# Optimization experiments

Hardware: AMD Instinct MI355X
Metric: run time of the kernel (lower is better)

## Reference

```python
import jax, jax.numpy as jnp
import numpy as np

B, T0, F, H, G = 32, 50, 171, 1024, 300


def _lstm_cell(x, h, c, Wih, Whh, bih, bhh):
    # PyTorch LSTMCell: gates ordered i, f, g, o
    gates = x @ Wih.T + bih + h @ Whh.T + bhh
    i, f, g, o = jnp.split(gates, 4, axis=-1)
    c_new = jax.nn.sigmoid(f) * c + jax.nn.sigmoid(i) * jnp.tanh(g)
    h_new = jax.nn.sigmoid(o) * jnp.tanh(c_new)
    return h_new, c_new


def setup_inputs() -> dict:
    key = jax.random.key(0)
    ks = jax.random.split(key, 16)
    s = 0.03  # small init to avoid gate saturation over 350 steps
    inp = {
        "initial_seq": jax.random.normal(ks[0], (B, T0, F), jnp.float32),
        "generate_frames_number": G,
        "Wih1": jax.random.normal(ks[1], (4 * H, F), jnp.float32) * s,
        "Whh1": jax.random.normal(ks[2], (4 * H, H), jnp.float32) * s,
        "bih1": jax.random.normal(ks[3], (4 * H,), jnp.float32) * s,
        "bhh1": jax.random.normal(ks[4], (4 * H,), jnp.float32) * s,
        "Wih2": jax.random.normal(ks[5], (4 * H, H), jnp.float32) * s,
        "Whh2": jax.random.normal(ks[6], (4 * H, H), jnp.float32) * s,
        "bih2": jax.random.normal(ks[7], (4 * H,), jnp.float32) * s,
        "bhh2": jax.random.normal(ks[8], (4 * H,), jnp.float32) * s,
        "Wih3": jax.random.normal(ks[9], (4 * H, H), jnp.float32) * s,
        "Whh3": jax.random.normal(ks[10], (4 * H, H), jnp.float32) * s,
        "bih3": jax.random.normal(ks[11], (4 * H,), jnp.float32) * s,
        "bhh3": jax.random.normal(ks[12], (4 * H,), jnp.float32) * s,
        "Wd": jax.random.normal(ks[13], (F, H), jnp.float32) * s,
        "bd": jax.random.normal(ks[14], (F,), jnp.float32) * s,
    }
    return inp


def _forward(initial_seq, gen_n,
             Wih1, Whh1, bih1, bhh1,
             Wih2, Whh2, bih2, bhh2,
             Wih3, Whh3, bih3, bhh3,
             Wd, bd):
    b = initial_seq.shape[0]
    z = jnp.zeros((b, H), initial_seq.dtype)

    def step(carry, in_frame):
        h0, h1, h2, c0, c1, c2 = carry
        # NOTE: faithful to original: lstm2/lstm3 consume the OLD h0/h1.
        nh0, nc0 = _lstm_cell(in_frame, h0, c0, Wih1, Whh1, bih1, bhh1)
        nh1, nc1 = _lstm_cell(h0, h1, c1, Wih2, Whh2, bih2, bhh2)
        nh2, nc2 = _lstm_cell(h1, h2, c2, Wih3, Whh3, bih3, bhh3)
        out_frame = nh2 @ Wd.T + bd
        return (nh0, nh1, nh2, nc0, nc1, nc2), out_frame

    # conditioned phase over the seed sequence
    carry = (z, z, z, z, z, z)
    carry, outs_cond = jax.lax.scan(step, carry, jnp.swapaxes(initial_seq, 0, 1))  # [T0,B,F]

    def gen_step(carry2, _):
        state, out_frame = carry2
        state, out_frame = step(state, out_frame)
        return (state, out_frame), out_frame

    (_, _), outs_gen = jax.lax.scan(gen_step, (carry, outs_cond[-1]), None, length=gen_n)

    outs = jnp.concatenate([outs_cond, outs_gen], axis=0)  # [T0+G, B, F]
    out_seq = jnp.swapaxes(outs, 0, 1).reshape(b, -1)      # [B, (T0+G)*F]
    original_seq = initial_seq.reshape(b, -1)              # [B, T0*F]
    return out_seq, original_seq


def reference(initial_seq, generate_frames_number,
              Wih1, Whh1, bih1, bhh1,
              Wih2, Whh2, bih2, bhh2,
              Wih3, Whh3, bih3, bhh3,
              Wd, bd):
    return _forward(initial_seq, generate_frames_number,
                    Wih1, Whh1, bih1, bhh1,
                    Wih2, Whh2, bih2, bhh2,
                    Wih3, Whh3, bih3, bhh3,
                    Wd, bd)
```

## Files before the change

### kernel.cpp

```cpp
#include <hip/hip_runtime.h>
#include <hip/hip_bf16.h>
#include <hip/hip_fp8.h>

#define Bn   32
#define Fdim 171
#define XPAD 256
#define Hdim 1024
#define NG   4096
#define K1K  1536
#define K1g  2048
#define K2c  2048
#define KDd  1024
#define WDR  176
#define NBLK 192
#define S1e  (80 * 512)
#define S2e  (128 * 512)

#define SW    64.0f
#define SA    16.0f
#define INVS  (1.0f / (SW * SA))

typedef __attribute__((ext_vector_type(4))) float f32x4;
typedef __attribute__((ext_vector_type(2))) long lx2;
typedef unsigned char fp8;

#define ALIGN256(x) ((((size_t)(x)) + 255) & ~(size_t)255)
constexpr size_t OFF_W1  = 0;
constexpr size_t OFF_W1G = ALIGN256(OFF_W1 + (size_t)NG * K1K);
constexpr size_t OFF_W2  = ALIGN256(OFF_W1G + (size_t)NG * K1g);
constexpr size_t OFF_W3  = ALIGN256(OFF_W2 + (size_t)NG * K2c);
constexpr size_t OFF_WD  = ALIGN256(OFF_W3 + (size_t)NG * K2c);
constexpr size_t OFF_B1  = ALIGN256(OFF_WD + (size_t)WDR * KDd);
constexpr size_t OFF_B1G = ALIGN256(OFF_B1 + (size_t)NG * 4);
constexpr size_t OFF_B2  = ALIGN256(OFF_B1G + (size_t)NG * 4);
constexpr size_t OFF_B3  = ALIGN256(OFF_B2 + (size_t)NG * 4);
constexpr size_t OFF_BD  = ALIGN256(OFF_B3 + (size_t)NG * 4);
constexpr size_t OFF_CB  = ALIGN256(OFF_BD + (size_t)WDR * 4);
constexpr size_t OFF_BAR = ALIGN256(OFF_CB + (size_t)3 * Bn * Hdim * 4);
constexpr size_t OFF_AB1 = ALIGN256(OFF_BAR + 16384);

#define FLG(i)   ((i) * 16)
#define LPW(l,m) (3072 + ((l) * 4 + (m)) * 16)

__device__ __forceinline__ int orig_row(int pr) {
    int u = pr >> 6, q = (pr >> 4) & 3, rr = pr & 15;
    return q * Hdim + u * 16 + rr;
}

__device__ __forceinline__ float sigm(float x) { return 1.f / (1.f + __expf(-x)); }
__device__ __forceinline__ float ftanh(float x) {
    float e = __expf(-2.f * fabsf(x));
    float t = (1.f - e) / (1.f + e);
    return x >= 0.f ? t : -t;
}

__device__ __forceinline__ unsigned char f2fp8(float x) {
    __hip_fp8_e4m3 q(x);
    return (unsigned char)q.__x;
}

__device__ __forceinline__ long ld8b(const fp8* p) {
    return *reinterpret_cast<const long*>(p);
}
__device__ __forceinline__ void st1c(fp8* p, unsigned char v) {
    __hip_atomic_store((unsigned char*)p, v, __ATOMIC_RELAXED, __HIP_MEMORY_SCOPE_AGENT);
}
__device__ __forceinline__ void stu64(unsigned long long* p, unsigned long long v) {
    __hip_atomic_store(p, v, __ATOMIC_RELAXED, __HIP_MEMORY_SCOPE_AGENT);
}
__device__ __forceinline__ unsigned ldflag(const unsigned* p) {
    return __hip_atomic_load(p, __ATOMIC_RELAXED, __HIP_MEMORY_SCOPE_AGENT);
}
__device__ __forceinline__ void stflag(unsigned* p, unsigned v) {
    __hip_atomic_store(p, v, __ATOMIC_RELAXED, __HIP_MEMORY_SCOPE_AGENT);
}
__device__ __forceinline__ f32x4 mfma8(long a, long b, f32x4 c) {
    return __builtin_amdgcn_mfma_f32_16x16x32_fp8_fp8(a, b, c, 0, 0, 0);
}

template <int NF>
__device__ __forceinline__ void aload(const fp8* __restrict__ As, int k0,
                                      int col, int kb8, long (&a0)[NF], long (&a1)[NF]) {
#pragma unroll
    for (int i = 0; i < NF; ++i) {
        int k = k0 + i * 32 + kb8;
        const fp8* ap = As + (size_t)(k >> 4) * 512 + (k & 15);
        a0[i] = ld8b(ap + col * 16);
        a1[i] = ld8b(ap + (col + 16) * 16);
    }
}

template <int NP>
__device__ __forceinline__ void wstream_pk(const fp8* __restrict__ wwave, int lane,
                                           const long (&a0)[2 * NP],
                                           const long (&a1)[2 * NP],
                                           f32x4 (&acc)[2][4]) {
#pragma unroll
    for (int i2 = 0; i2 < NP; ++i2) {
        const fp8* p = wwave + i2 * 4096 + lane * 16;
#pragma unroll
        for (int q = 0; q < 4; ++q) {
            lx2 wv = *reinterpret_cast<const lx2*>(p + q * 1024);
            acc[0][q] = mfma8(a0[2 * i2],     wv[0], acc[0][q]);
            acc[1][q] = mfma8(a1[2 * i2],     wv[0], acc[1][q]);
            acc[0][q] = mfma8(a0[2 * i2 + 1], wv[1], acc[0][q]);
            acc[1][q] = mfma8(a1[2 * i2 + 1], wv[1], acc[1][q]);
        }
    }
}

__global__ void k_pack_pk(int mode, const float* Wih, const float* Whh,
                          const float* Wd, fp8* dst, int Kpk) {
    const size_t n = (size_t)NG * Kpk;
    const int kq = Kpk >> 3;
    for (size_t idx = (size_t)blockIdx.x * blockDim.x + threadIdx.x; idx < n;
         idx += (size_t)gridDim.x * blockDim.x) {
        int ut = (int)(idx / ((size_t)64 * Kpk));
        int rem = (int)(idx % ((size_t)64 * Kpk));
        int w = rem / (8 * Kpk);
        int rem2 = rem % (8 * Kpk);
        int i2 = rem2 >> 12;
        int q = (rem2 >> 10) & 3;
        int lane = (rem2 >> 4) & 63;
        int b = rem2 & 15;
        int ro = orig_row(ut * 64 + q * 16 + (lane & 15));
        int k = w * kq + (2 * i2 + (b >> 3)) * 32 + ((lane >> 4) << 3) + (b & 7);
        float v = 0.f;
        if (mode == 0) {
            if (k < Fdim) v = Wih[(size_t)ro * Fdim + k];
            else if (k >= XPAD && k < XPAD + Hdim) v = Whh[(size_t)ro * Hdim + (k - XPAD)];
        } else if (mode == 1) {
            if (k < Hdim) {
                float a = 0.f;
                for (int f = 0; f < Fdim; ++f)
                    a += Wih[(size_t)ro * Fdim + f] * Wd[(size_t)f * KDd + k];
                v = a;
            } else {
                v = Whh[(size_t)ro * Hdim + (k - Hdim)];
            }
        } else {
            v = (k < Hdim) ? Wih[(size_t)ro * Hdim + k]
                           : Whh[(size_t)ro * Hdim + (k - Hdim)];
        }
        dst[idx] = f2fp8(v * SW);
    }
}

__global__ void k_pack_wd(const float* Wd, fp8* dst) {
    const size_t n = (size_t)WDR * KDd;
    for (size_t i = (size_t)blockIdx.x * blockDim.x + threadIdx.x; i < n;
         i += (size_t)gridDim.x * blockDim.x) {
        int r = (int)(i / KDd), k = (int)(i % KDd);
        float v = (r < Fdim) ? Wd[(size_t)r * KDd + k] : 0.f;
        dst[i] = f2fp8(v * SW);
    }
}

__global__ void k_pack_bias(const float* bi1, const float* bh1,
                            const float* bi2, const float* bh2,
                            const float* bi3, const float* bh3,
                            const float* bd,
                            float* B1, float* B2, float* B3, float* BD) {
    const int n = 3 * NG + WDR;
    for (int i = blockIdx.x * blockDim.x + threadIdx.x; i < n;
         i += gridDim.x * blockDim.x) {
        if (i < NG)            { int ro = orig_row(i);        B1[i]        = bi1[ro] + bh1[ro]; }
        else if (i < 2 * NG)   { int ro = orig_row(i - NG);   B2[i - NG]   = bi2[ro] + bh2[ro]; }
        else if (i < 3 * NG)   { int ro = orig_row(i - 2*NG); B3[i - 2*NG] = bi3[ro] + bh3[ro]; }
        else { int r = i - 3 * NG; BD[r] = (r < Fdim) ? bd[r] : 0.f; }
    }
}

__global__ void k_pack_b1g(const float* bi1, const float* bh1,
                           const float* Wih, const float* bd, float* B1G) {
    for (int pr = blockIdx.x * blockDim.x + threadIdx.x; pr < NG;
         pr += gridDim.x * blockDim.x) {
        int ro = orig_row(pr);
        float acc = bi1[ro] + bh1[ro];
        for (int f = 0; f < Fdim; ++f)
            acc += Wih[(size_t)ro * Fdim + f] * bd[f];
        B1G[pr] = acc;
    }
}

__global__ void k_init(fp8* ab1, fp8* ab2, fp8* ab3, float* cb, unsigned* bar, int D) {
    const size_t n1 = (size_t)D * (S1e / 8);
    const size_t n2 = (size_t)D * (S2e / 8);
    const size_t nc = 3 * Bn * Hdim;
    const size_t tot = n1 + 2 * n2 + nc + 4096;
    for (size_t i = (size_t)blockIdx.x * blockDim.x + threadIdx.x; i < tot;
         i += (size_t)gridDim.x * blockDim.x) {
        if (i < n1)             stu64((unsigned long long*)ab1 + i, 0ull);
        else if (i < n1 + n2)   stu64((unsigned long long*)ab2 + (i - n1), 0ull);
        else if (i < n1 + 2*n2) stu64((unsigned long long*)ab3 + (i - n1 - n2), 0ull);
        else if (i < n1 + 2*n2 + nc) cb[i - n1 - 2*n2] = 0.f;
        else bar[i - n1 - 2*n2 - nc] = 0u;
    }
}

__global__ void k_stage0(const float* xseq, fp8* ab1, int T0) {
    for (int idx = blockIdx.x * blockDim.x + threadIdx.x; idx < Bn * 11 * 16;
         idx += gridDim.x * blockDim.x) {
        int fu = idx >> 9, rem = idx & 511, b = rem >> 4, jj = rem & 15;
        int f = fu * 16 + jj;
        if (f < Fdim)
            st1c(&ab1[idx], f2fp8(xseq[(size_t)b * T0 * Fdim + f] * SA));
    }
}

__global__ void k_copy_orig(const float* xseq, float* out, int T, int T0) {
    const int n = Bn * T0 * Fdim;
    const size_t base = (size_t)Bn * T * Fdim;
    for (int i = blockIdx.x * blockDim.x + threadIdx.x; i < n;
         i += gridDim.x * blockDim.x) {
        out[base + i] = xseq[i];
    }
}

__device__ __forceinline__ void pollLP(unsigned* bar, int la, int lb,
                                       unsigned tgt, int lane, int m) {
    for (;;) {
        bool ok = true;
        if (lane == 0) ok = (ldflag(&bar[LPW(la, m)]) >= tgt);
        else if (lane == 1 && lb >= 0) ok = (ldflag(&bar[LPW(lb, m)]) >= tgt);
        if (__all(ok)) break;
        __builtin_amdgcn_s_sleep(1);
    }
    asm volatile("" ::: "memory");
}

__global__ __launch_bounds__(512, 1) void k_lstm(
    const float* __restrict__ xseq, float* __restrict__ out,
    const fp8* __restrict__ W1, const fp8* __restrict__ W1G,
    const fp8* __restrict__ W2, const fp8* __restrict__ W3,
    const fp8* __restrict__ WD,
    const float* __restrict__ b1, const float* __restrict__ b1g,
    const float* __restrict__ b2, const float* __restrict__ b3,
    const float* __restrict__ bdp,
    fp8* ab1, fp8* ab2, fp8* ab3, float* cb,
    unsigned* bar, int T0, int T, int dm) {
    __shared__ float red[8][32][66];
    __shared__ fp8 hstage[512];
    __shared__ fp8 xstage[5632];

    const int tid = threadIdx.x;
    const int w = tid >> 6;
    const int lane = tid & 63;
    const int bid = blockIdx.x;

    if (bid == NBLK) {
        if (w < 3) {
            unsigned tgt = 1;
            const unsigned* fp = &bar[FLG(64 * w + lane)];
            while (tgt <= (unsigned)T) {
                unsigned v = ldflag(fp);
                if (__all(v >= tgt)) {
                    if (lane < 4) stflag(&bar[LPW(w, lane)], tgt);
                    ++tgt;
                } else {
                    __builtin_amdgcn_s_sleep(1);
                }
            }
        }
        return;
    }

    const int col = lane & 15;
    const int kb8 = (lane >> 4) << 3;
    const int layer = bid >> 6;
    const int ut = bid & 63;
    const bool isdec = (bid >= 64 && bid < 75);
    const int dnt = bid - 64;

    const int eb = w + 8 * (lane >> 4);
    const int ejj = lane & 15;
    const int off = eb * 16 + ejj;

    fp8* dst0s = (layer == 0) ? ab1 : (layer == 1) ? ab2 : ab3;
    const size_t d0off = (layer == 0) ? (size_t)(16 + ut) * 512
                                      : (size_t)(64 + ut) * 512;
    const size_t d0slot = (layer == 0) ? (size_t)S1e : (size_t)S2e;
    fp8* dst1s = (layer == 0) ? ab2 : (layer == 1) ? ab3 : nullptr;
    const size_t d1off = (size_t)ut * 512;

    for (int t = 0; t < T; ++t) {
        const int st = t & dm;
        const int ns = (t + 1) & dm;

        if (w == 0) {
            int la, lb = -1;
            if (layer == 0) { if (t < T0) { la = 0; } else { la = 2; lb = 0; } }
            else if (layer == 1) { la = 0; lb = 1; }
            else { la = 1; lb = 2; }
            pollLP(bar, la, lb, (unsigned)t, lane, bid & 3);
        }
        __syncthreads();

        f32x4 acc[2][4] = {};
        if (layer == 0) {
            if (t < T0) {
                const fp8* As = ab1 + (size_t)st * S1e;
                long a0[6], a1[6];
                aload<6>(As, w * (K1K / 8), col, kb8, a0, a1);
                wstream_pk<3>(W1 + (size_t)ut * 64 * K1K + (size_t)w * 8 * K1K,
                              lane, a0, a1, acc);
            } else {
                const fp8* Ah = (w < 4) ? ab3 + (size_t)st * S2e + 64 * 512
                                        : ab1 + (size_t)st * S1e + 16 * 512;
                long a0[8], a1[8];
                aload<8>(Ah, (w & 3) * 256, col, kb8, a0, a1);
                wstream_pk<4>(W1G + (size_t)ut * 64 * K1g + (size_t)w * 8 * K1g,
                              lane, a0, a1, acc);
            }
        } else if (layer == 1) {
            const fp8* As = ab2 + (size_t)st * S2e;
            long a0[8], a1[8];
            aload<8>(As, w * 256, col, kb8, a0, a1);
            wstream_pk<4>(W2 + (size_t)ut * 64 * K2c + (size_t)w * 8 * K2c,
                          lane, a0, a1, acc);
        } else {
            const fp8* As = ab3 + (size_t)st * S2e;
            long a0[8], a1[8];
            aload<8>(As, w * 256, col, kb8, a0, a1);
            wstream_pk<4>(W3 + (size_t)ut * 64 * K2c + (size_t)w * 8 * K2c,
                          lane, a0, a1, acc);
        }

        __syncthreads();
#pragma unroll
        for (int mt = 0; mt < 2; ++mt)
#pragma unroll
            for (int q = 0; q < 4; ++q)
#pragma unroll
                for (int r = 0; r < 4; ++r)
                    red[w][mt * 16 + (lane >> 4) * 4 + r][q * 16 + col] = acc[mt][q][r];
        __syncthreads();

        {
            const float* bl = (layer == 0) ? ((t >= T0) ? b1g : b1)
                                           : (layer == 1) ? b2 : b3;
            float s[4];
#pragma unroll
            for (int q = 0; q < 4; ++q) {
                float a = 0.f;
#pragma unroll
                for (int ww = 0; ww < 8; ++ww) a += red[ww][eb][q * 16 + ejj];
                s[q] = a * INVS + bl[ut * 64 + q * 16 + ejj];
            }
            size_t cidx = ((size_t)layer * Bn + eb) * Hdim + ut * 16 + ejj;
            float cold = cb[cidx];
            float cn = sigm(s[1]) * cold + sigm(s[0]) * ftanh(s[2]);
            float hn = sigm(s[3]) * ftanh(cn);
            cb[cidx] = cn;
            hstage[off] = f2fp8(hn * SA);
        }

        if (bid == 11 && t + 1 < T0) {
            for (int idx = tid; idx < Bn * 11 * 16; idx += 512) {
                int fu = idx >> 9, rem = idx & 511, b = rem >> 4, jj = rem & 15;
                int f = fu * 16 + jj;
                xstage[idx] = (f < Fdim)
                    ? f2fp8(xseq[((size_t)b * T0 + t + 1) * Fdim + f] * SA)
                    : (fp8)0;
            }
        }

        __syncthreads();

        if (tid < 64) {
            unsigned long long v =
                *reinterpret_cast<unsigned long long*>(&hstage[tid * 8]);
            stu64((unsigned long long*)(dst0s + (size_t)ns * d0slot + d0off + tid * 8), v);
        } else if (tid < 128 && dst1s != nullptr) {
            unsigned long long v =
                *reinterpret_cast<unsigned long long*>(&hstage[(tid - 64) * 8]);
            stu64((unsigned long long*)(dst1s + (size_t)ns * S2e + d1off + (tid - 64) * 8), v);
        }
        if (bid == 11 && t + 1 < T0 && tid < 128) {
            fp8* dst = ab1 + (size_t)ns * S1e;
            for (int i8 = tid; i8 < 704; i8 += 128) {
                unsigned long long v =
                    *reinterpret_cast<unsigned long long*>(&xstage[i8 * 8]);
                stu64((unsigned long long*)(dst + i8 * 8), v);
            }
        }

        __syncthreads();
        if (tid == 0) stflag(&bar[FLG(bid)], (unsigned)(t + 1));

        if (isdec) {
            if (w == 0) pollLP(bar, 2, -1, (unsigned)(t + 1), lane, bid & 3);
            __syncthreads();
            const fp8* Ad = ab3 + (size_t)ns * S2e + 64 * 512;
            const fp8* Wrowd = WD + (size_t)(dnt * 16) * KDd;
            long d0[4], d1[4];
            aload<4>(Ad, w * 128, col, kb8, d0, d1);
            f32x4 dacc[2] = {};
#pragma unroll
            for (int i = 0; i < 4; ++i) {
                long bq = ld8b(Wrowd + (size_t)col * KDd + w * 128 + i * 32 + kb8);
                dacc[0] = mfma8(d0[i], bq, dacc[0]);
                dacc[1] = mfma8(d1[i], bq, dacc[1]);
            }
            __syncthreads();
#pragma unroll
            for (int mt = 0; mt < 2; ++mt)
#pragma unroll
                for (int r = 0; r < 4; ++r)
                    red[w][mt * 16 + (lane >> 4) * 4 + r][col] = dacc[mt][r];
            __syncthreads();
            {
                int f = dnt * 16 + ejj;
                float v = 0.f;
#pragma unroll
                for (int ww = 0; ww < 8; ++ww) v += red[ww][eb][ejj];
                v = v * INVS + bdp[f];
                if (f < Fdim)
                    out[(size_t)eb * ((size_t)T * Fdim) + (size_t)t * Fdim + f] = v;
            }
        }
    }
}

extern "C" void kernel_launch(void* const* d_in, const int* in_sizes, int n_in,
                              void* d_out, int out_size, void* d_ws, size_t ws_size,
                              hipStream_t stream) {
    const float* xseq = (const float*)d_in[0];
    const float* Wih1 = (const float*)d_in[2];
    const float* Whh1 = (const float*)d_in[3];
    const float* bih1 = (const float*)d_in[4];
    const float* bhh1 = (const float*)d_in[5];
    const float* Wih2 = (const float*)d_in[6];
    const float* Whh2 = (const float*)d_in[7];
    const float* bih2 = (const float*)d_in[8];
    const float* bhh2 = (const float*)d_in[9];
    const float* Wih3 = (const float*)d_in[10];
    const float* Whh3 = (const float*)d_in[11];
    const float* bih3 = (const float*)d_in[12];
    const float* bhh3 = (const float*)d_in[13];
    const float* Wd   = (const float*)d_in[14];
    const float* bd   = (const float*)d_in[15];

    const int T0 = in_sizes[0] / (Bn * Fdim);
    const int T  = out_size / (Bn * Fdim) - T0;

    char* ws = (char*)d_ws;
    fp8*   pW1  = (fp8*)(ws + OFF_W1);
    fp8*   pW1G = (fp8*)(ws + OFF_W1G);
    fp8*   pW2  = (fp8*)(ws + OFF_W2);
    fp8*   pW3  = (fp8*)(ws + OFF_W3);
    fp8*   pWD  = (fp8*)(ws + OFF_WD);
    float* pB1  = (float*)(ws + OFF_B1);
    float* pB1G = (float*)(ws + OFF_B1G);
    float* pB2  = (float*)(ws + OFF_B2);
    float* pB3  = (float*)(ws + OFF_B3);
    float* pBD  = (float*)(ws + OFF_BD);
    float* cbp  = (float*)(ws + OFF_CB);
    unsigned* bar = (unsigned*)(ws + OFF_BAR);
    float* out = (float*)d_out;

    int D = 32;
    while (D > 4 &&
           OFF_AB1 + (size_t)D * ((size_t)S1e + 2 * (size_t)S2e) > ws_size)
        D >>= 1;
    fp8* ab1 = (fp8*)(ws + OFF_AB1);
    fp8* ab2 = ab1 + (size_t)D * S1e;
    fp8* ab3 = ab2 + (size_t)D * S2e;

    (void)n_in;

    hipLaunchKernelGGL(k_pack_pk, dim3(1024), dim3(256), 0, stream,
                       0, Wih1, Whh1, Wd, pW1, K1K);
    hipLaunchKernelGGL(k_pack_pk, dim3(4096), dim3(256), 0, stream,
                       1, Wih1, Whh1, Wd, pW1G, K1g);
    hipLaunchKernelGGL(k_pack_pk, dim3(1024), dim3(256), 0, stream,
                       2, Wih2, Whh2, Wd, pW2, K2c);
    hipLaunchKernelGGL(k_pack_pk, dim3(1024), dim3(256), 0, stream,
                       2, Wih3, Whh3, Wd, pW3, K2c);
    hipLaunchKernelGGL(k_pack_wd, dim3(704), dim3(256), 0, stream, Wd, pWD);
    hipLaunchKernelGGL(k_pack_bias, dim3(49), dim3(256), 0, stream,
                       bih1, bhh1, bih2, bhh2, bih3, bhh3, bd, pB1, pB2, pB3, pBD);
    hipLaunchKernelGGL(k_pack_b1g, dim3(16), dim3(256), 0, stream,
                       bih1, bhh1, Wih1, bd, pB1G);
    hipLaunchKernelGGL(k_init, dim3(2048), dim3(256), 0, stream,
                       ab1, ab2, ab3, cbp, bar, D);
    hipLaunchKernelGGL(k_stage0, dim3(22), dim3(256), 0, stream, xseq, ab1, T0);
    hipLaunchKernelGGL(k_lstm, dim3(NBLK + 1), dim3(512), 0, stream,
                       xseq, out, pW1, pW1G, pW2, pW3, pWD,
                       pB1, pB1G, pB2, pB3, pBD,
                       ab1, ab2, ab3, cbp, bar, T0, T, D - 1);
    hipLaunchKernelGGL(k_copy_orig, dim3(1069), dim3(256), 0, stream, xseq, out, T, T0);
}
```

Measured before the change: 2.570 ms.

## Replace aggregator-block barrier with direct per-wave polling of producer flags

Removes the dedicated aggregator block that collected per-block step flags and republished per-layer flags. Each wave now polls the specific producer block flags it depends on, with adaptive sleep backoff, and most block-wide __syncthreads around polling are dropped. The writer wave issues its stores, waits on vmcnt, then sets the flag itself. This removes one hop of flag latency per step but adds more polling traffic on the flags, and relies on a per-wave vmcnt wait for ordering between the data stores and the flag store.

```diff
diff --git a/kernel.cpp b/kernel.cpp
--- a/kernel.cpp
+++ b/kernel.cpp
@@ -40,7 +40,6 @@
 constexpr size_t OFF_AB1 = ALIGN256(OFF_BAR + 16384);
 
 #define FLG(i)   ((i) * 16)
-#define LPW(l,m) (3072 + ((l) * 4 + (m)) * 16)
 
 __device__ __forceinline__ int orig_row(int pr) {
     int u = pr >> 6, q = (pr >> 4) & 3, rr = pr & 15;
@@ -76,6 +75,19 @@
 }
 __device__ __forceinline__ f32x4 mfma8(long a, long b, f32x4 c) {
     return __builtin_amdgcn_mfma_f32_16x16x32_fp8_fp8(a, b, c, 0, 0, 0);
+}
+
+__device__ __forceinline__ void polladapt(unsigned* bar, int idx, unsigned tgt) {
+    int tries = 0;
+    for (;;) {
+        bool ok = true;
+        if (idx >= 0) ok = (ldflag(&bar[FLG(idx)]) >= tgt);
+        if (__all(ok)) break;
+        if (tries < 4) __builtin_amdgcn_s_sleep(1);
+        else           __builtin_amdgcn_s_sleep(8);
+        ++tries;
+    }
+    asm volatile("" ::: "memory");
 }
 
 template <int NF>
@@ -136,7 +148,7 @@
                     a += Wih[(size_t)ro * Fdim + f] * Wd[(size_t)f * KDd + k];
                 v = a;
             } else {
-                v = Whh[(size_t)ro * Hdim + (k - Hdim)];
+                v = Whh[(size_t)ro * Hdim + (k - 1024)];
             }
         } else {
             v = (k < Hdim) ? Wih[(size_t)ro * Hdim + k]
@@ -215,18 +227,6 @@
          i += gridDim.x * blockDim.x) {
         out[base + i] = xseq[i];
     }
-}
-
-__device__ __forceinline__ void pollLP(unsigned* bar, int la, int lb,
-                                       unsigned tgt, int lane, int m) {
-    for (;;) {
-        bool ok = true;
-        if (lane == 0) ok = (ldflag(&bar[LPW(la, m)]) >= tgt);
-        else if (lane == 1 && lb >= 0) ok = (ldflag(&bar[LPW(lb, m)]) >= tgt);
-        if (__all(ok)) break;
-        __builtin_amdgcn_s_sleep(1);
-    }
-    asm volatile("" ::: "memory");
 }
 
 __global__ __launch_bounds__(512, 1) void k_lstm(
@@ -247,24 +247,6 @@
     const int w = tid >> 6;
     const int lane = tid & 63;
     const int bid = blockIdx.x;
-
-    if (bid == NBLK) {
-        if (w < 3) {
-            unsigned tgt = 1;
-            const unsigned* fp = &bar[FLG(64 * w + lane)];
-            while (tgt <= (unsigned)T) {
-                unsigned v = ldflag(fp);
-                if (__all(v >= tgt)) {
-                    if (lane < 4) stflag(&bar[LPW(w, lane)], tgt);
-                    ++tgt;
-                } else {
-                    __builtin_amdgcn_s_sleep(1);
-                }
-            }
-        }
-        return;
-    }
-
     const int col = lane & 15;
     const int kb8 = (lane >> 4) << 3;
     const int layer = bid >> 6;
@@ -283,42 +265,44 @@
     fp8* dst1s = (layer == 0) ? ab2 : (layer == 1) ? ab3 : nullptr;
     const size_t d1off = (size_t)ut * 512;
 
+    int gpidx = -1;
+    if (lane < 16) {
+        if (layer == 0)      gpidx = (w < 4) ? 128 + 16 * w + lane : 16 * (w - 4) + lane;
+        else if (layer == 1) gpidx = (w < 4) ? 16 * w + lane : 64 + 16 * (w - 4) + lane;
+        else                 gpidx = (w < 4) ? 64 + 16 * w + lane : 128 + 16 * (w - 4) + lane;
+    }
+    int cpidx = (layer == 0) ? lane : gpidx;
+
     for (int t = 0; t < T; ++t) {
         const int st = t & dm;
         const int ns = (t + 1) & dm;
 
-        if (w == 0) {
-            int la, lb = -1;
-            if (layer == 0) { if (t < T0) { la = 0; } else { la = 2; lb = 0; } }
-            else if (layer == 1) { la = 0; lb = 1; }
-            else { la = 1; lb = 2; }
-            pollLP(bar, la, lb, (unsigned)t, lane, bid & 3);
-        }
-        __syncthreads();
-
         f32x4 acc[2][4] = {};
-        if (layer == 0) {
-            if (t < T0) {
-                const fp8* As = ab1 + (size_t)st * S1e;
-                long a0[6], a1[6];
-                aload<6>(As, w * (K1K / 8), col, kb8, a0, a1);
-                wstream_pk<3>(W1 + (size_t)ut * 64 * K1K + (size_t)w * 8 * K1K,
-                              lane, a0, a1, acc);
-            } else {
-                const fp8* Ah = (w < 4) ? ab3 + (size_t)st * S2e + 64 * 512
-                                        : ab1 + (size_t)st * S1e + 16 * 512;
-                long a0[8], a1[8];
-                aload<8>(Ah, (w & 3) * 256, col, kb8, a0, a1);
-                wstream_pk<4>(W1G + (size_t)ut * 64 * K1g + (size_t)w * 8 * K1g,
-                              lane, a0, a1, acc);
-            }
+        if (layer == 0 && t < T0) {
+            if (w == 0) polladapt(bar, cpidx, (unsigned)t);
+            __syncthreads();
+            const fp8* As = ab1 + (size_t)st * S1e;
+            long a0[6], a1[6];
+            aload<6>(As, w * (K1K / 8), col, kb8, a0, a1);
+            wstream_pk<3>(W1 + (size_t)ut * 64 * K1K + (size_t)w * 8 * K1K,
+                          lane, a0, a1, acc);
+        } else if (layer == 0) {
+            polladapt(bar, gpidx, (unsigned)t);
+            const fp8* Ah = (w < 4) ? ab3 + (size_t)st * S2e + 64 * 512
+                                    : ab1 + (size_t)st * S1e + 16 * 512;
+            long a0[8], a1[8];
+            aload<8>(Ah, (w & 3) * 256, col, kb8, a0, a1);
+            wstream_pk<4>(W1G + (size_t)ut * 64 * K1g + (size_t)w * 8 * K1g,
+                          lane, a0, a1, acc);
         } else if (layer == 1) {
+            polladapt(bar, gpidx, (unsigned)t);
             const fp8* As = ab2 + (size_t)st * S2e;
             long a0[8], a1[8];
             aload<8>(As, w * 256, col, kb8, a0, a1);
             wstream_pk<4>(W2 + (size_t)ut * 64 * K2c + (size_t)w * 8 * K2c,
                           lane, a0, a1, acc);
         } else {
+            polladapt(bar, gpidx, (unsigned)t);
             const fp8* As = ab3 + (size_t)st * S2e;
             long a0[8], a1[8];
             aload<8>(As, w * 256, col, kb8, a0, a1);
@@ -367,30 +351,27 @@
 
         __syncthreads();
 
-        if (tid < 64) {
+        if (w == 0) {
             unsigned long long v =
-                *reinterpret_cast<unsigned long long*>(&hstage[tid * 8]);
-            stu64((unsigned long long*)(dst0s + (size_t)ns * d0slot + d0off + tid * 8), v);
-        } else if (tid < 128 && dst1s != nullptr) {
-            unsigned long long v =
-                *reinterpret_cast<unsigned long long*>(&hstage[(tid - 64) * 8]);
-            stu64((unsigned long long*)(dst1s + (size_t)ns * S2e + d1off + (tid - 64) * 8), v);
-        }
-        if (bid == 11 && t + 1 < T0 && tid < 128) {
-            fp8* dst = ab1 + (size_t)ns * S1e;
-            for (int i8 = tid; i8 < 704; i8 += 128) {
-                unsigned long long v =
-                    *reinterpret_cast<unsigned long long*>(&xstage[i8 * 8]);
-                stu64((unsigned long long*)(dst + i8 * 8), v);
-            }
-        }
-
-        __syncthreads();
-        if (tid == 0) stflag(&bar[FLG(bid)], (unsigned)(t + 1));
+                *reinterpret_cast<unsigned long long*>(&hstage[lane * 8]);
+            stu64((unsigned long long*)(dst0s + (size_t)ns * d0slot + d0off + lane * 8), v);
+            if (dst1s != nullptr)
+                stu64((unsigned long long*)(dst1s + (size_t)ns * S2e + d1off + lane * 8), v);
+            if (bid == 11 && t + 1 < T0) {
+                fp8* dst = ab1 + (size_t)ns * S1e;
+                for (int i8 = lane; i8 < 704; i8 += 64) {
+                    unsigned long long xv =
+                        *reinterpret_cast<unsigned long long*>(&xstage[i8 * 8]);
+                    stu64((unsigned long long*)(dst + i8 * 8), xv);
+                }
+            }
+            asm volatile("s_waitcnt vmcnt(0)" ::: "memory");
+            if (lane == 0) stflag(&bar[FLG(bid)], (unsigned)(t + 1));
+        }
 
         if (isdec) {
-            if (w == 0) pollLP(bar, 2, -1, (unsigned)(t + 1), lane, bid & 3);
-            __syncthreads();
+            int dpidx = (lane < 8) ? 128 + 8 * w + lane : -1;
+            polladapt(bar, dpidx, (unsigned)(t + 1));
             const fp8* Ad = ab3 + (size_t)ns * S2e + 64 * 512;
             const fp8* Wrowd = WD + (size_t)(dnt * 16) * KDd;
             long d0[4], d1[4];
@@ -485,7 +466,7 @@
     hipLaunchKernelGGL(k_init, dim3(2048), dim3(256), 0, stream,
                        ab1, ab2, ab3, cbp, bar, D);
     hipLaunchKernelGGL(k_stage0, dim3(22), dim3(256), 0, stream, xseq, ab1, T0);
-    hipLaunchKernelGGL(k_lstm, dim3(NBLK + 1), dim3(512), 0, stream,
+    hipLaunchKernelGGL(k_lstm, dim3(NBLK), dim3(512), 0, stream,
                        xseq, out, pW1, pW1G, pW2, pW3, pWD,
                        pB1, pB1G, pB2, pB3, pBD,
                        ab1, ab2, ab3, cbp, bar, T0, T, D - 1);
```

After: 2.656 ms. 3.3% more time.

## Split LSTM work across 384 smaller blocks and move decoder into dedicated blocks

Applied to the files above, without the earlier changes.

Changes the persistent LSTM kernel from 192 blocks of 512 threads, each owning 16 hidden units, to 384 blocks of 256 threads, each owning 8 units, with the weight packing and bias ordering adjusted to match. The output projection moves out of the layer-2 worker blocks into 11 separate decoder blocks, so workers no longer stall on the decoder each step. The barrier monitor now covers 128 blocks per layer and publishes 8 mirrored flags, and the poll loop backs off with longer sleeps. The aim is to spread the per-step weight streaming over more compute units and take the decoder off the recurrent critical path. The cost is more blocks to synchronise and more per-wave register pressure, since each wave holds 16 A fragments.

```diff
diff --git a/kernel.cpp b/kernel.cpp
--- a/kernel.cpp
+++ b/kernel.cpp
@@ -12,7 +12,9 @@
 #define K2c  2048
 #define KDd  1024
 #define WDR  176
-#define NBLK 192
+#define BPL  128
+#define NWRK (3 * BPL)
+#define NDEC 11
 #define S1e  (80 * 512)
 #define S2e  (128 * 512)
 
@@ -37,14 +39,14 @@
 constexpr size_t OFF_BD  = ALIGN256(OFF_B3 + (size_t)NG * 4);
 constexpr size_t OFF_CB  = ALIGN256(OFF_BD + (size_t)WDR * 4);
 constexpr size_t OFF_BAR = ALIGN256(OFF_CB + (size_t)3 * Bn * Hdim * 4);
-constexpr size_t OFF_AB1 = ALIGN256(OFF_BAR + 16384);
+constexpr size_t OFF_AB1 = ALIGN256(OFF_BAR + 32768);
 
 #define FLG(i)   ((i) * 16)
-#define LPW(l,m) (3072 + ((l) * 4 + (m)) * 16)
-
-__device__ __forceinline__ int orig_row(int pr) {
-    int u = pr >> 6, q = (pr >> 4) & 3, rr = pr & 15;
-    return q * Hdim + u * 16 + rr;
+#define LPW(l,m) (6144 + ((l) * 8 + (m)) * 16)
+
+__device__ __forceinline__ int orig_row2(int pr) {
+    int ut2 = pr >> 5, g = (pr >> 3) & 3, u = pr & 7;
+    return g * 1024 + ut2 * 8 + u;
 }
 
 __device__ __forceinline__ float sigm(float x) { return 1.f / (1.f + __expf(-x)); }
@@ -78,6 +80,21 @@
     return __builtin_amdgcn_mfma_f32_16x16x32_fp8_fp8(a, b, c, 0, 0, 0);
 }
 
+__device__ __forceinline__ void pollLP(unsigned* bar, int la, int lb,
+                                       unsigned tgt, int lane, int m) {
+    int tries = 0;
+    for (;;) {
+        bool ok = true;
+        if (lane == 0) ok = (ldflag(&bar[LPW(la, m)]) >= tgt);
+        else if (lane == 1 && lb >= 0) ok = (ldflag(&bar[LPW(lb, m)]) >= tgt);
+        if (__all(ok)) break;
+        if (tries < 4) __builtin_amdgcn_s_sleep(1);
+        else           __builtin_amdgcn_s_sleep(4);
+        ++tries;
+    }
+    asm volatile("" ::: "memory");
+}
+
 template <int NF>
 __device__ __forceinline__ void aload(const fp8* __restrict__ As, int k0,
                                       int col, int kb8, long (&a0)[NF], long (&a1)[NF]) {
@@ -94,17 +111,17 @@
 __device__ __forceinline__ void wstream_pk(const fp8* __restrict__ wwave, int lane,
                                            const long (&a0)[2 * NP],
                                            const long (&a1)[2 * NP],
-                                           f32x4 (&acc)[2][4]) {
+                                           f32x4 (&acc)[2][2]) {
 #pragma unroll
     for (int i2 = 0; i2 < NP; ++i2) {
-        const fp8* p = wwave + i2 * 4096 + lane * 16;
-#pragma unroll
-        for (int q = 0; q < 4; ++q) {
-            lx2 wv = *reinterpret_cast<const lx2*>(p + q * 1024);
-            acc[0][q] = mfma8(a0[2 * i2],     wv[0], acc[0][q]);
-            acc[1][q] = mfma8(a1[2 * i2],     wv[0], acc[1][q]);
-            acc[0][q] = mfma8(a0[2 * i2 + 1], wv[1], acc[0][q]);
-            acc[1][q] = mfma8(a1[2 * i2 + 1], wv[1], acc[1][q]);
+        const fp8* p = wwave + i2 * 2048 + lane * 16;
+#pragma unroll
+        for (int q2 = 0; q2 < 2; ++q2) {
+            lx2 wv = *reinterpret_cast<const lx2*>(p + q2 * 1024);
+            acc[0][q2] = mfma8(a0[2 * i2],     wv[0], acc[0][q2]);
+            acc[1][q2] = mfma8(a1[2 * i2],     wv[0], acc[1][q2]);
+            acc[0][q2] = mfma8(a0[2 * i2 + 1], wv[1], acc[0][q2]);
+            acc[1][q2] = mfma8(a1[2 * i2 + 1], wv[1], acc[1][q2]);
         }
     }
 }
@@ -112,18 +129,20 @@
 __global__ void k_pack_pk(int mode, const float* Wih, const float* Whh,
                           const float* Wd, fp8* dst, int Kpk) {
     const size_t n = (size_t)NG * Kpk;
-    const int kq = Kpk >> 3;
+    const int kq = Kpk >> 2;
     for (size_t idx = (size_t)blockIdx.x * blockDim.x + threadIdx.x; idx < n;
          idx += (size_t)gridDim.x * blockDim.x) {
-        int ut = (int)(idx / ((size_t)64 * Kpk));
-        int rem = (int)(idx % ((size_t)64 * Kpk));
+        int ut2 = (int)(idx / ((size_t)32 * Kpk));
+        int rem = (int)(idx % ((size_t)32 * Kpk));
         int w = rem / (8 * Kpk);
         int rem2 = rem % (8 * Kpk);
-        int i2 = rem2 >> 12;
-        int q = (rem2 >> 10) & 3;
+        int i2 = rem2 >> 11;
+        int q2 = (rem2 >> 10) & 1;
         int lane = (rem2 >> 4) & 63;
         int b = rem2 & 15;
-        int ro = orig_row(ut * 64 + q * 16 + (lane & 15));
+        int rr = lane & 15;
+        int g = q2 * 2 + (rr >> 3), u = rr & 7;
+        int ro = g * 1024 + ut2 * 8 + u;
         int k = w * kq + (2 * i2 + (b >> 3)) * 32 + ((lane >> 4) << 3) + (b & 7);
         float v = 0.f;
         if (mode == 0) {
@@ -136,7 +155,7 @@
                     a += Wih[(size_t)ro * Fdim + f] * Wd[(size_t)f * KDd + k];
                 v = a;
             } else {
-                v = Whh[(size_t)ro * Hdim + (k - Hdim)];
+                v = Whh[(size_t)ro * Hdim + (k - 1024)];
             }
         } else {
             v = (k < Hdim) ? Wih[(size_t)ro * Hdim + k]
@@ -164,9 +183,9 @@
     const int n = 3 * NG + WDR;
     for (int i = blockIdx.x * blockDim.x + threadIdx.x; i < n;
          i += gridDim.x * blockDim.x) {
-        if (i < NG)            { int ro = orig_row(i);        B1[i]        = bi1[ro] + bh1[ro]; }
-        else if (i < 2 * NG)   { int ro = orig_row(i - NG);   B2[i - NG]   = bi2[ro] + bh2[ro]; }
-        else if (i < 3 * NG)   { int ro = orig_row(i - 2*NG); B3[i - 2*NG] = bi3[ro] + bh3[ro]; }
+        if (i < NG)            { int ro = orig_row2(i);        B1[i]        = bi1[ro] + bh1[ro]; }
+        else if (i < 2 * NG)   { int ro = orig_row2(i - NG);   B2[i - NG]   = bi2[ro] + bh2[ro]; }
+        else if (i < 3 * NG)   { int ro = orig_row2(i - 2*NG); B3[i - 2*NG] = bi3[ro] + bh3[ro]; }
         else { int r = i - 3 * NG; BD[r] = (r < Fdim) ? bd[r] : 0.f; }
     }
 }
@@ -175,7 +194,7 @@
                            const float* Wih, const float* bd, float* B1G) {
     for (int pr = blockIdx.x * blockDim.x + threadIdx.x; pr < NG;
          pr += gridDim.x * blockDim.x) {
-        int ro = orig_row(pr);
+        int ro = orig_row2(pr);
         float acc = bi1[ro] + bh1[ro];
         for (int f = 0; f < Fdim; ++f)
             acc += Wih[(size_t)ro * Fdim + f] * bd[f];
@@ -187,7 +206,7 @@
     const size_t n1 = (size_t)D * (S1e / 8);
     const size_t n2 = (size_t)D * (S2e / 8);
     const size_t nc = 3 * Bn * Hdim;
-    const size_t tot = n1 + 2 * n2 + nc + 4096;
+    const size_t tot = n1 + 2 * n2 + nc + 8192;
     for (size_t i = (size_t)blockIdx.x * blockDim.x + threadIdx.x; i < tot;
          i += (size_t)gridDim.x * blockDim.x) {
         if (i < n1)             stu64((unsigned long long*)ab1 + i, 0ull);
@@ -217,19 +236,7 @@
     }
 }
 
-__device__ __forceinline__ void pollLP(unsigned* bar, int la, int lb,
-                                       unsigned tgt, int lane, int m) {
-    for (;;) {
-        bool ok = true;
-        if (lane == 0) ok = (ldflag(&bar[LPW(la, m)]) >= tgt);
-        else if (lane == 1 && lb >= 0) ok = (ldflag(&bar[LPW(lb, m)]) >= tgt);
-        if (__all(ok)) break;
-        __builtin_amdgcn_s_sleep(1);
-    }
-    asm volatile("" ::: "memory");
-}
-
-__global__ __launch_bounds__(512, 1) void k_lstm(
+__global__ __launch_bounds__(256, 2) void k_lstm(
     const float* __restrict__ xseq, float* __restrict__ out,
     const fp8* __restrict__ W1, const fp8* __restrict__ W1G,
     const fp8* __restrict__ W2, const fp8* __restrict__ W3,
@@ -239,23 +246,26 @@
     const float* __restrict__ bdp,
     fp8* ab1, fp8* ab2, fp8* ab3, float* cb,
     unsigned* bar, int T0, int T, int dm) {
-    __shared__ float red[8][32][66];
-    __shared__ fp8 hstage[512];
+    __shared__ float red[4][32][34];
+    __shared__ fp8 hstage[256];
     __shared__ fp8 xstage[5632];
 
     const int tid = threadIdx.x;
     const int w = tid >> 6;
     const int lane = tid & 63;
     const int bid = blockIdx.x;
-
-    if (bid == NBLK) {
+    const int col = lane & 15;
+    const int kb8 = (lane >> 4) << 3;
+
+    if (bid == NWRK + NDEC) {
         if (w < 3) {
             unsigned tgt = 1;
-            const unsigned* fp = &bar[FLG(64 * w + lane)];
+            const unsigned* f0 = &bar[FLG(w * BPL + lane)];
+            const unsigned* f1 = &bar[FLG(w * BPL + 64 + lane)];
             while (tgt <= (unsigned)T) {
-                unsigned v = ldflag(fp);
-                if (__all(v >= tgt)) {
-                    if (lane < 4) stflag(&bar[LPW(w, lane)], tgt);
+                unsigned v0 = ldflag(f0), v1 = ldflag(f1);
+                if (__all(v0 >= tgt && v1 >= tgt)) {
+                    if (lane < 8) stflag(&bar[LPW(w, lane)], tgt);
                     ++tgt;
                 } else {
                     __builtin_amdgcn_s_sleep(1);
@@ -265,64 +275,95 @@
         return;
     }
 
-    const int col = lane & 15;
-    const int kb8 = (lane >> 4) << 3;
-    const int layer = bid >> 6;
-    const int ut = bid & 63;
-    const bool isdec = (bid >= 64 && bid < 75);
-    const int dnt = bid - 64;
-
-    const int eb = w + 8 * (lane >> 4);
-    const int ejj = lane & 15;
-    const int off = eb * 16 + ejj;
+    const int mir = bid & 7;
+
+    if (bid >= NWRK) {
+        const int dnt = bid - NWRK;
+        const fp8* Wrowd = WD + (size_t)(dnt * 16) * KDd;
+        for (int t = 0; t < T; ++t) {
+            const int ns = (t + 1) & dm;
+            pollLP(bar, 2, -1, (unsigned)(t + 1), lane, mir);
+            const fp8* Ad = ab3 + (size_t)ns * S2e + 64 * 512;
+            long d0[8], d1[8];
+            aload<8>(Ad, w * 256, col, kb8, d0, d1);
+            f32x4 dacc[2] = {};
+#pragma unroll
+            for (int i = 0; i < 8; ++i) {
+                long bq = ld8b(Wrowd + (size_t)col * KDd + w * 256 + i * 32 + kb8);
+                dacc[0] = mfma8(d0[i], bq, dacc[0]);
+                dacc[1] = mfma8(d1[i], bq, dacc[1]);
+            }
+            __syncthreads();
+#pragma unroll
+            for (int mt = 0; mt < 2; ++mt)
+#pragma unroll
+                for (int r = 0; r < 4; ++r)
+                    red[w][mt * 16 + (lane >> 4) * 4 + r][col] = dacc[mt][r];
+            __syncthreads();
+#pragma unroll
+            for (int h = 0; h < 2; ++h) {
+                int idx = h * 256 + tid;
+                int b = idx >> 4, jj = idx & 15;
+                int f = dnt * 16 + jj;
+                float v = 0.f;
+#pragma unroll
+                for (int ww = 0; ww < 4; ++ww) v += red[ww][b][jj];
+                v = v * INVS + bdp[f];
+                if (f < Fdim)
+                    out[(size_t)b * ((size_t)T * Fdim) + (size_t)t * Fdim + f] = v;
+            }
+            __syncthreads();
+        }
+        return;
+    }
+
+    const int layer = bid >> 7;
+    const int ut2 = bid & 127;
+
+    const int eb = tid >> 3;
+    const int eu = tid & 7;
 
     fp8* dst0s = (layer == 0) ? ab1 : (layer == 1) ? ab2 : ab3;
-    const size_t d0off = (layer == 0) ? (size_t)(16 + ut) * 512
-                                      : (size_t)(64 + ut) * 512;
+    const size_t d0off = ((layer == 0) ? (size_t)(16 + (ut2 >> 1))
+                                       : (size_t)(64 + (ut2 >> 1))) * 512 +
+                         (size_t)(ut2 & 1) * 8;
     const size_t d0slot = (layer == 0) ? (size_t)S1e : (size_t)S2e;
     fp8* dst1s = (layer == 0) ? ab2 : (layer == 1) ? ab3 : nullptr;
-    const size_t d1off = (size_t)ut * 512;
+    const size_t d1off = (size_t)(ut2 >> 1) * 512 + (size_t)(ut2 & 1) * 8;
 
     for (int t = 0; t < T; ++t) {
         const int st = t & dm;
         const int ns = (t + 1) & dm;
 
-        if (w == 0) {
-            int la, lb = -1;
-            if (layer == 0) { if (t < T0) { la = 0; } else { la = 2; lb = 0; } }
-            else if (layer == 1) { la = 0; lb = 1; }
-            else { la = 1; lb = 2; }
-            pollLP(bar, la, lb, (unsigned)t, lane, bid & 3);
-        }
-        __syncthreads();
-
-        f32x4 acc[2][4] = {};
-        if (layer == 0) {
-            if (t < T0) {
-                const fp8* As = ab1 + (size_t)st * S1e;
-                long a0[6], a1[6];
-                aload<6>(As, w * (K1K / 8), col, kb8, a0, a1);
-                wstream_pk<3>(W1 + (size_t)ut * 64 * K1K + (size_t)w * 8 * K1K,
-                              lane, a0, a1, acc);
-            } else {
-                const fp8* Ah = (w < 4) ? ab3 + (size_t)st * S2e + 64 * 512
-                                        : ab1 + (size_t)st * S1e + 16 * 512;
-                long a0[8], a1[8];
-                aload<8>(Ah, (w & 3) * 256, col, kb8, a0, a1);
-                wstream_pk<4>(W1G + (size_t)ut * 64 * K1g + (size_t)w * 8 * K1g,
-                              lane, a0, a1, acc);
-            }
+        f32x4 acc[2][2] = {};
+        if (layer == 0 && t < T0) {
+            pollLP(bar, 0, -1, (unsigned)t, lane, mir);
+            const fp8* As = ab1 + (size_t)st * S1e;
+            long a0[12], a1[12];
+            aload<12>(As, w * 384, col, kb8, a0, a1);
+            wstream_pk<6>(W1 + (size_t)ut2 * 32 * K1K + (size_t)w * 8 * K1K,
+                          lane, a0, a1, acc);
+        } else if (layer == 0) {
+            pollLP(bar, 2, 0, (unsigned)t, lane, mir);
+            const fp8* Ah = (w < 2) ? ab3 + (size_t)st * S2e + 64 * 512
+                                    : ab1 + (size_t)st * S1e + 16 * 512;
+            long a0[16], a1[16];
+            aload<16>(Ah, (w & 1) * 512, col, kb8, a0, a1);
+            wstream_pk<8>(W1G + (size_t)ut2 * 32 * K1g + (size_t)w * 8 * K1g,
+                          lane, a0, a1, acc);
         } else if (layer == 1) {
+            pollLP(bar, 0, 1, (unsigned)t, lane, mir);
             const fp8* As = ab2 + (size_t)st * S2e;
-            long a0[8], a1[8];
-            aload<8>(As, w * 256, col, kb8, a0, a1);
-            wstream_pk<4>(W2 + (size_t)ut * 64 * K2c + (size_t)w * 8 * K2c,
+            long a0[16], a1[16];
+            aload<16>(As, w * 512, col, kb8, a0, a1);
+            wstream_pk<8>(W2 + (size_t)ut2 * 32 * K2c + (size_t)w * 8 * K2c,
                           lane, a0, a1, acc);
         } else {
+            pollLP(bar, 1, 2, (unsigned)t, lane, mir);
             const fp8* As = ab3 + (size_t)st * S2e;
-            long a0[8], a1[8];
-            aload<8>(As, w * 256, col, kb8, a0, a1);
-            wstream_pk<4>(W3 + (size_t)ut * 64 * K2c + (size_t)w * 8 * K2c,
+            long a0[16], a1[16];
+            aload<16>(As, w * 512, col, kb8, a0, a1);
+            wstream_pk<8>(W3 + (size_t)ut2 * 32 * K2c + (size_t)w * 8 * K2c,
                           lane, a0, a1, acc);
         }
 
@@ -330,10 +371,10 @@
 #pragma unroll
         for (int mt = 0; mt < 2; ++mt)
 #pragma unroll
-            for (int q = 0; q < 4; ++q)
+            for (int q2 = 0; q2 < 2; ++q2)
 #pragma unroll
                 for (int r = 0; r < 4; ++r)
-                    red[w][mt * 16 + (lane >> 4) * 4 + r][q * 16 + col] = acc[mt][q][r];
+                    red[w][mt * 16 + (lane >> 4) * 4 + r][q2 * 16 + col] = acc[mt][q2][r];
         __syncthreads();
 
         {
@@ -341,22 +382,22 @@
                                            : (layer == 1) ? b2 : b3;
             float s[4];
 #pragma unroll
-            for (int q = 0; q < 4; ++q) {
+            for (int g = 0; g < 4; ++g) {
                 float a = 0.f;
 #pragma unroll
-                for (int ww = 0; ww < 8; ++ww) a += red[ww][eb][q * 16 + ejj];
-                s[q] = a * INVS + bl[ut * 64 + q * 16 + ejj];
-            }
-            size_t cidx = ((size_t)layer * Bn + eb) * Hdim + ut * 16 + ejj;
+                for (int ww = 0; ww < 4; ++ww) a += red[ww][eb][g * 8 + eu];
+                s[g] = a * INVS + bl[ut2 * 32 + g * 8 + eu];
+            }
+            size_t cidx = ((size_t)layer * Bn + eb) * Hdim + ut2 * 8 + eu;
             float cold = cb[cidx];
             float cn = sigm(s[1]) * cold + sigm(s[0]) * ftanh(s[2]);
             float hn = sigm(s[3]) * ftanh(cn);
             cb[cidx] = cn;
-            hstage[off] = f2fp8(hn * SA);
+            hstage[eb * 8 + eu] = f2fp8(hn * SA);
         }
 
         if (bid == 11 && t + 1 < T0) {
-            for (int idx = tid; idx < Bn * 11 * 16; idx += 512) {
+            for (int idx = tid; idx < Bn * 11 * 16; idx += 256) {
                 int fu = idx >> 9, rem = idx & 511, b = rem >> 4, jj = rem & 15;
                 int f = fu * 16 + jj;
                 xstage[idx] = (f < Fdim)
@@ -367,58 +408,27 @@
 
         __syncthreads();
 
-        if (tid < 64) {
+        if (tid < 32) {
             unsigned long long v =
                 *reinterpret_cast<unsigned long long*>(&hstage[tid * 8]);
-            stu64((unsigned long long*)(dst0s + (size_t)ns * d0slot + d0off + tid * 8), v);
-        } else if (tid < 128 && dst1s != nullptr) {
+            stu64((unsigned long long*)(dst0s + (size_t)ns * d0slot + d0off + (size_t)tid * 16), v);
+        } else if (tid < 64 && dst1s != nullptr) {
+            int b = tid - 32;
             unsigned long long v =
-                *reinterpret_cast<unsigned long long*>(&hstage[(tid - 64) * 8]);
-            stu64((unsigned long long*)(dst1s + (size_t)ns * S2e + d1off + (tid - 64) * 8), v);
-        }
-        if (bid == 11 && t + 1 < T0 && tid < 128) {
+                *reinterpret_cast<unsigned long long*>(&hstage[b * 8]);
+            stu64((unsigned long long*)(dst1s + (size_t)ns * S2e + d1off + (size_t)b * 16), v);
+        }
+        if (bid == 11 && t + 1 < T0) {
             fp8* dst = ab1 + (size_t)ns * S1e;
-            for (int i8 = tid; i8 < 704; i8 += 128) {
-                unsigned long long v =
+            for (int i8 = tid; i8 < 704; i8 += 256) {
+                unsigned long long xv =
                     *reinterpret_cast<unsigned long long*>(&xstage[i8 * 8]);
-                stu64((unsigned long long*)(dst + i8 * 8), v);
+                stu64((unsigned long long*)(dst + i8 * 8), xv);
             }
         }
 
         __syncthreads();
         if (tid == 0) stflag(&bar[FLG(bid)], (unsigned)(t + 1));
-
-        if (isdec) {
-            if (w == 0) pollLP(bar, 2, -1, (unsigned)(t + 1), lane, bid & 3);
-            __syncthreads();
-            const fp8* Ad = ab3 + (size_t)ns * S2e + 64 * 512;
-            const fp8* Wrowd = WD + (size_t)(dnt * 16) * KDd;
-            long d0[4], d1[4];
-            aload<4>(Ad, w * 128, col, kb8, d0, d1);
-            f32x4 dacc[2] = {};
-#pragma unroll
-            for (int i = 0; i < 4; ++i) {
-                long bq = ld8b(Wrowd + (size_t)col * KDd + w * 128 + i * 32 + kb8);
-                dacc[0] = mfma8(d0[i], bq, dacc[0]);
-                dacc[1] = mfma8(d1[i], bq, dacc[1]);
-            }
-            __syncthreads();
-#pragma unroll
-            for (int mt = 0; mt < 2; ++mt)
-#pragma unroll
-                for (int r = 0; r < 4; ++r)
-                    red[w][mt * 16 + (lane >> 4) * 4 + r][col] = dacc[mt][r];
-            __syncthreads();
-            {
-                int f = dnt * 16 + ejj;
-                float v = 0.f;
-#pragma unroll
-                for (int ww = 0; ww < 8; ++ww) v += red[ww][eb][ejj];
-                v = v * INVS + bdp[f];
-                if (f < Fdim)
-                    out[(size_t)eb * ((size_t)T * Fdim) + (size_t)t * Fdim + f] = v;
-            }
-        }
     }
 }
 
@@ -485,7 +495,7 @@
     hipLaunchKernelGGL(k_init, dim3(2048), dim3(256), 0, stream,
                        ab1, ab2, ab3, cbp, bar, D);
     hipLaunchKernelGGL(k_stage0, dim3(22), dim3(256), 0, stream, xseq, ab1, T0);
-    hipLaunchKernelGGL(k_lstm, dim3(NBLK + 1), dim3(512), 0, stream,
+    hipLaunchKernelGGL(k_lstm, dim3(NWRK + NDEC + 1), dim3(256), 0, stream,
                        xseq, out, pW1, pW1G, pW2, pW3, pWD,
                        pB1, pB1G, pB2, pB3, pBD,
                        ab1, ab2, ab3, cbp, bar, T0, T, D - 1);
```

Result: slower. 2.924 ms (+13.8%).
